# Kernel optimization log

Measured on AMD Instinct MI355X. Metric: run time of the kernel, lower is better.

## Reference

```python
import jax, jax.numpy as jnp
import numpy as np

B, S, E, H, NL = 64, 256, 1024, 16, 2
D = E // H          # head dim = 64
FF = 4 * E          # 4096
EPS = 1e-5
MASKED = -10000.0   # masked_bias buffer value


def layer_norm(x, g, b):
    m = jnp.mean(x, axis=-1, keepdims=True)
    v = jnp.mean(jnp.square(x - m), axis=-1, keepdims=True)
    return (x - m) * jax.lax.rsqrt(v + EPS) * g + b


def setup_inputs() -> dict:
    key = jax.random.key(0)
    ks = jax.random.split(key, 8)
    s = 0.02
    return {
        "sentence_hidden": jax.random.normal(ks[0], (B, S, E), dtype=jnp.float32),
        "wpe": jax.random.normal(ks[1], (256, E), dtype=jnp.float32) * s,
        "ln1_g": jnp.ones((NL, E), jnp.float32),
        "ln1_b": jnp.zeros((NL, E), jnp.float32),
        "attn_w": jax.random.normal(ks[2], (NL, E, 3 * E), dtype=jnp.float32) * s,
        "attn_b": jnp.zeros((NL, 3 * E), jnp.float32),
        "attn_proj_w": jax.random.normal(ks[3], (NL, E, E), dtype=jnp.float32) * s,
        "attn_proj_b": jnp.zeros((NL, E), jnp.float32),
        "ln2_g": jnp.ones((NL, E), jnp.float32),
        "ln2_b": jnp.zeros((NL, E), jnp.float32),
        "fc_w": jax.random.normal(ks[4], (NL, E, FF), dtype=jnp.float32) * s,
        "fc_b": jnp.zeros((NL, FF), jnp.float32),
        "mlp_proj_w": jax.random.normal(ks[5], (NL, FF, E), dtype=jnp.float32) * s,
        "mlp_proj_b": jnp.zeros((NL, E), jnp.float32),
        "lnf_g": jnp.ones((E,), jnp.float32),
        "lnf_b": jnp.zeros((E,), jnp.float32),
    }


def reference(sentence_hidden, wpe, ln1_g, ln1_b, attn_w, attn_b, attn_proj_w,
              attn_proj_b, ln2_g, ln2_b, fc_w, fc_b, mlp_proj_w, mlp_proj_b,
              lnf_g, lnf_b):
    # position embeddings: positions 0..S-1 (wpe has 256 rows, S == 256)
    h = sentence_hidden + wpe[:S][None, :, :]
    causal = jnp.tril(jnp.ones((S, S), dtype=bool))  # [S,S]
    scale = 1.0 / np.sqrt(D)
    for i in range(NL):
        # --- attention ---
        x = layer_norm(h, ln1_g[i], ln1_b[i])
        qkv = x @ attn_w[i] + attn_b[i]                    # [B,S,3E]
        q, k, v = jnp.split(qkv, 3, axis=-1)
        q = q.reshape(B, S, H, D).transpose(0, 2, 1, 3)    # [B,H,S,D]
        k = k.reshape(B, S, H, D).transpose(0, 2, 1, 3)
        v = v.reshape(B, S, H, D).transpose(0, 2, 1, 3)
        w = jnp.einsum("bhqd,bhkd->bhqk", q, k) * scale    # [B,H,S,S]
        w = jnp.where(causal, w, jnp.asarray(MASKED, w.dtype))
        w = jax.nn.softmax(w, axis=-1)
        a = jnp.einsum("bhqk,bhkd->bhqd", w, v)            # [B,H,S,D]
        a = a.transpose(0, 2, 1, 3).reshape(B, S, E)
        a = a @ attn_proj_w[i] + attn_proj_b[i]
        h = h + a
        # --- MLP ---
        x = layer_norm(h, ln2_g[i], ln2_b[i])
        m = jax.nn.gelu(x @ fc_w[i] + fc_b[i], approximate=True)  # gelu_new
        m = m @ mlp_proj_w[i] + mlp_proj_b[i]
        h = h + m
    h = layer_norm(h, lnf_g, lnf_b)
    loss = jnp.mean(jnp.square(h[0, :-1, :] - sentence_hidden[0, 1:, :]))
    return (h, loss)
```

## Files before the change

kernel.cpp:

```cpp
#include <hip/hip_runtime.h>
#include <cstdint>
#include <cstddef>


typedef __attribute__((ext_vector_type(4))) float f32x4;
typedef __attribute__((ext_vector_type(16))) float f32x16;
typedef __attribute__((ext_vector_type(8))) __bf16 bf16x8;
typedef __attribute__((ext_vector_type(4))) unsigned int u32x4;
typedef __attribute__((ext_vector_type(8))) unsigned short u16x8;
typedef __attribute__((ext_vector_type(4))) unsigned short u16x4;

__device__ __forceinline__ unsigned short f2bf(float x) {
  unsigned int u = __builtin_bit_cast(unsigned int, x);
  u += 0x7fffu + ((u >> 16) & 1u);
  return (unsigned short)(u >> 16);
}
__device__ __forceinline__ float gelu_new(float x) {
  float u = 0.7978845608028654f * (x + 0.044715f * x * x * x);
  return x * __builtin_amdgcn_rcpf(1.0f + __expf(-2.0f * u));
}
__device__ __forceinline__ unsigned int cvtpk(float lo, float hi) {
  unsigned int r;
  asm("v_cvt_pk_bf16_f32 %0, %1, %2" : "=v"(r) : "v"(lo), "v"(hi));
  return r;
}
__device__ __forceinline__ void plswap(unsigned int& a, unsigned int& b) {
  asm("v_permlane32_swap_b32 %0, %1" : "+v"(a), "+v"(b));
}

__global__ __launch_bounds__(256) void transpose_bf16(
    const float* __restrict__ W, unsigned short* __restrict__ Wt, int K, int N) {
  __shared__ float tile[32][33];
  const int n0 = blockIdx.x * 32, k0 = blockIdx.y * 32;
  const int tx = threadIdx.x, ty = threadIdx.y;
#pragma unroll
  for (int j = 0; j < 32; j += 8)
    tile[ty + j][tx] = W[(size_t)(k0 + ty + j) * N + n0 + tx];
  __syncthreads();
#pragma unroll
  for (int j = 0; j < 32; j += 8)
    Wt[(size_t)(n0 + ty + j) * K + k0 + tx] = f2bf(tile[tx][ty + j]);
}

__device__ __forceinline__ void ln_core(
    f32x4 v, const float* g, const float* bb, int row, int t,
    int outf32, void* outp) {
  float s = v.x + v.y + v.z + v.w;
  float sq = v.x * v.x + v.y * v.y + v.z * v.z + v.w * v.w;
#pragma unroll
  for (int off = 32; off; off >>= 1) {
    s += __shfl_xor(s, off, 64);
    sq += __shfl_xor(sq, off, 64);
  }
  __shared__ float red[8];
  if ((t & 63) == 0) { red[t >> 6] = s; red[4 + (t >> 6)] = sq; }
  __syncthreads();
  s = red[0] + red[1] + red[2] + red[3];
  sq = red[4] + red[5] + red[6] + red[7];
  const float mean = s * (1.0f / 1024.0f);
  const float var = sq * (1.0f / 1024.0f) - mean * mean;
  const float rs = rsqrtf(var + 1e-5f);
  const f32x4 gv = ((const f32x4*)g)[t];
  const f32x4 bv = ((const f32x4*)bb)[t];
  float y0 = (v.x - mean) * rs * gv.x + bv.x;
  float y1 = (v.y - mean) * rs * gv.y + bv.y;
  float y2 = (v.z - mean) * rs * gv.z + bv.z;
  float y3 = (v.w - mean) * rs * gv.w + bv.w;
  if (outf32) {
    f32x4 o; o.x = y0; o.y = y1; o.z = y2; o.w = y3;
    ((f32x4*)outp)[(size_t)row * 256 + t] = o;
  } else {
    u16x4 pk;
    pk.x = f2bf(y0); pk.y = f2bf(y1); pk.z = f2bf(y2); pk.w = f2bf(y3);
    ((u16x4*)outp)[(size_t)row * 256 + t] = pk;
  }
}

template <int OUTF32>
__global__ __launch_bounds__(256) void ln_kernel(
    const float* __restrict__ hin, const float* __restrict__ g,
    const float* __restrict__ bb, void* __restrict__ outp) {
  const int row = blockIdx.x, t = threadIdx.x;
  const f32x4 v = ((const f32x4*)(hin + (size_t)row * 1024))[t];
  ln_core(v, g, bb, row, t, OUTF32, outp);
}

__global__ __launch_bounds__(256) void ln_wpe_kernel(
    const float* __restrict__ sent, const float* __restrict__ wpe,
    const float* __restrict__ g, const float* __restrict__ bb,
    float* __restrict__ h, unsigned short* __restrict__ xb) {
  const int row = blockIdx.x, t = threadIdx.x;
  const int s = row & 255;
  f32x4 a = ((const f32x4*)(sent + (size_t)row * 1024))[t];
  f32x4 w = ((const f32x4*)(wpe + (size_t)s * 1024))[t];
  f32x4 v = a + w;
  ((f32x4*)(h + (size_t)row * 1024))[t] = v;
  ln_core(v, g, bb, row, t, 0, xb);
}

template <int EPI>
__global__ __launch_bounds__(512, 2) void gemmp(
    const unsigned short* __restrict__ A, const unsigned short* __restrict__ Bt,
    const float* __restrict__ bias, unsigned short* __restrict__ Cb,
    float* __restrict__ Hres, int N, int K, int gx, int gy) {
  constexpr int A_E = 16384;
  constexpr int BUF_E = A_E + 16384;
  __shared__ alignas(16) unsigned short smem[2 * BUF_E];

  const int nwg = gx * gy;
  const int dd = blockIdx.x;
  const int wrk = (dd & 7) * (nwg >> 3) + (dd >> 3);
  const int grp = wrk / (gx * 4);
  const int r = wrk - grp * (gx * 4);
  const int bx = r >> 2;
  const int by = grp * 4 + (r & 3);
  const int row0 = by * 256, col0 = bx * 256;

  const int t = threadIdx.x;
  const int wid = t >> 6, l = t & 63;
  const int wm = wid >> 2, wn = wid & 3;
  const int fr = l & 15, q4 = l >> 4;

  const int cx0 = (q4 ^ (fr & 7)) * 8;
  const int cx1 = ((4 + q4) ^ (fr & 7)) * 8;
  const int b_r0 = (wn * 64 + fr) * 64;
  auto a_slot = [&](int m) -> int { return (wm * 128 + m * 16 + fr) * 64; };

  const int lrow = l >> 3;
  const int scol = ((l & 7) ^ (lrow & 7)) * 8;

  auto stB = [&](int tt, int win) {
    const unsigned short* s =
        Bt + (size_t)(col0 + win * 8 + lrow) * K + tt * 64 + scol;
    __builtin_amdgcn_global_load_lds(
        (const __attribute__((address_space(1))) void*)s,
        (__attribute__((address_space(3))) void*)(smem + (tt & 1) * BUF_E + A_E + win * 512),
        16, 0, 0);
  };
  auto stA = [&](int tt, int win) {
    const unsigned short* s =
        A + (size_t)(row0 + win * 8 + lrow) * K + tt * 64 + scol;
    __builtin_amdgcn_global_load_lds(
        (const __attribute__((address_space(1))) void*)s,
        (__attribute__((address_space(3))) void*)(smem + (tt & 1) * BUF_E + win * 512),
        16, 0, 0);
  };
  auto stageB_set = [&](int tt) {
    stB(tt, 2 * wid); stB(tt, 2 * wid + 1);
    stB(tt, 16 + 2 * wid); stB(tt, 16 + 2 * wid + 1);
  };
  auto stageA_set = [&](int tt) {
    const int i0 = 2 * wid, i1 = 2 * wid + 1;
    stA(tt, i0 < 8 ? i0 : 8 + i0);
    stA(tt, i1 < 8 ? i1 : 8 + i1);
    stA(tt, i0 < 8 ? 8 + i0 : 16 + i0);
    stA(tt, i1 < 8 ? 8 + i1 : 16 + i1);
  };

  const int nt = K >> 6;

  stageB_set(0);
  stageA_set(0);
  asm volatile("s_waitcnt vmcnt(2)" ::: "memory");
  __builtin_amdgcn_s_barrier();
  asm volatile("" ::: "memory");

  f32x4 acc[8][4];
#pragma unroll
  for (int m = 0; m < 8; ++m)
#pragma unroll
    for (int n = 0; n < 4; ++n) {
      acc[m][n].x = 0.f; acc[m][n].y = 0.f; acc[m][n].z = 0.f; acc[m][n].w = 0.f;
    }

  for (int tc = 0; tc < nt; ++tc) {
    const unsigned short* Ab = smem + (tc & 1) * BUF_E;
    const unsigned short* Bb = Ab + A_E;
    const bool pf = (tc + 1) < nt;

    bf16x8 b0[4], b1[4], a0[4], a1[4];
#pragma unroll
    for (int n = 0; n < 4; ++n) b0[n] = *(const bf16x8*)(Bb + b_r0 + n * 1024 + cx0);
#pragma unroll
    for (int m = 0; m < 4; ++m) a0[m] = *(const bf16x8*)(Ab + a_slot(m) + cx0);
#pragma unroll
    for (int n = 0; n < 4; ++n) b1[n] = *(const bf16x8*)(Bb + b_r0 + n * 1024 + cx1);
#pragma unroll
    for (int m = 0; m < 4; ++m) a1[m] = *(const bf16x8*)(Ab + a_slot(m) + cx1);

    if (pf) stageB_set(tc + 1);

    __builtin_amdgcn_s_setprio(1);
#pragma unroll
    for (int m = 0; m < 4; ++m)
#pragma unroll
      for (int n = 0; n < 4; ++n)
        acc[m][n] = __builtin_amdgcn_mfma_f32_16x16x32_bf16(a0[m], b0[n], acc[m][n], 0, 0, 0);
    __builtin_amdgcn_s_setprio(0);

    if (pf) stageA_set(tc + 1);

    __builtin_amdgcn_s_setprio(1);
#pragma unroll
    for (int m = 0; m < 4; ++m)
#pragma unroll
      for (int n = 0; n < 4; ++n)
        acc[m][n] = __builtin_amdgcn_mfma_f32_16x16x32_bf16(a1[m], b1[n], acc[m][n], 0, 0, 0);
    __builtin_amdgcn_s_setprio(0);

    if (pf) asm volatile("s_waitcnt vmcnt(8)" ::: "memory");
    else    asm volatile("s_waitcnt vmcnt(0)" ::: "memory");
    __builtin_amdgcn_s_barrier();
    asm volatile("" ::: "memory");

    bf16x8 h0[4], h1[4];
#pragma unroll
    for (int m = 0; m < 4; ++m) h0[m] = *(const bf16x8*)(Ab + a_slot(4 + m) + cx0);
#pragma unroll
    for (int m = 0; m < 4; ++m) h1[m] = *(const bf16x8*)(Ab + a_slot(4 + m) + cx1);

    __builtin_amdgcn_s_setprio(1);
#pragma unroll
    for (int m = 0; m < 4; ++m)
#pragma unroll
      for (int n = 0; n < 4; ++n)
        acc[4 + m][n] = __builtin_amdgcn_mfma_f32_16x16x32_bf16(h0[m], b0[n], acc[4 + m][n], 0, 0, 0);
    __builtin_amdgcn_s_setprio(0);
    __builtin_amdgcn_s_setprio(1);
#pragma unroll
    for (int m = 0; m < 4; ++m)
#pragma unroll
      for (int n = 0; n < 4; ++n)
        acc[4 + m][n] = __builtin_amdgcn_mfma_f32_16x16x32_bf16(h1[m], b1[n], acc[4 + m][n], 0, 0, 0);
    __builtin_amdgcn_s_setprio(0);

    if (pf) asm volatile("s_waitcnt vmcnt(2)" ::: "memory");
    else    asm volatile("s_waitcnt vmcnt(0)" ::: "memory");
    __builtin_amdgcn_s_barrier();
    asm volatile("" ::: "memory");
  }

  if constexpr (EPI == 2) {
#pragma unroll
    for (int n = 0; n < 4; ++n) {
      const int col = col0 + wn * 64 + n * 16 + fr;
      const float bi = bias[col];
#pragma unroll
      for (int m = 0; m < 8; ++m)
#pragma unroll
        for (int e = 0; e < 4; ++e) {
          const int row = row0 + wm * 128 + m * 16 + q4 * 4 + e;
          Hres[(size_t)row * N + col] += acc[m][n][e] + bi;
        }
    }
  } else {
    char* wreg = (char*)smem + wid * 9216;
    float bi[4];
#pragma unroll
    for (int n = 0; n < 4; ++n) bi[n] = bias[col0 + wn * 64 + n * 16 + fr];
#pragma unroll
    for (int half = 0; half < 2; ++half) {
#pragma unroll
      for (int m = 0; m < 4; ++m)
#pragma unroll
        for (int n = 0; n < 4; ++n)
#pragma unroll
          for (int e = 0; e < 4; ++e) {
            float v = acc[half * 4 + m][n][e] + bi[n];
            if (EPI == 1) v = gelu_new(v);
            *(unsigned short*)(wreg + (m * 16 + q4 * 4 + e) * 144 +
                               (n * 16 + fr) * 2) = f2bf(v);
          }
#pragma unroll
      for (int rb = 0; rb < 8; ++rb) {
        const int rowl = rb * 8 + (l >> 3);
        u16x8 vv = *(const u16x8*)(wreg + rowl * 144 + (l & 7) * 16);
        const int rg = row0 + wm * 128 + half * 64 + rowl;
        *(u16x8*)(Cb + (size_t)rg * N + col0 + wn * 64 + (l & 7) * 8) = vv;
      }
    }
  }
}

__global__ __launch_bounds__(256) void attn_mfma(
    const unsigned short* __restrict__ qkv, unsigned short* __restrict__ aout,
    int b0) {
  __shared__ alignas(16) unsigned short Klds[256 * 64];
  __shared__ alignas(16) unsigned short Vt[64 * 256];
  const int bh = blockIdx.x;
  const int bl = bh >> 4, hd = bh & 15;
  const size_t base = (size_t)bl * 256 * 3072 + (size_t)hd * 64;
  const int t = threadIdx.x;
  const int w = t >> 6, l = t & 63;
  const int lq = l & 31, hl = l >> 5;

#pragma unroll
  for (int i = 0; i < 8; ++i) {
    const int r = i * 32 + (t >> 3);
    const int c = t & 7;
    u16x8 kv = *(const u16x8*)(qkv + base + (size_t)r * 3072 + 1024 + c * 8);
    *(u16x8*)(Klds + r * 64 + ((c ^ (r & 7)) * 8)) = kv;
    u16x8 vv = *(const u16x8*)(qkv + base + (size_t)r * 3072 + 2048 + c * 8);
#pragma unroll
    for (int j = 0; j < 8; ++j) {
      const int d = c * 8 + j;
      Vt[d * 256 + (((r >> 3) ^ (d & 31)) * 8) + (r & 7)] = vv[j];
    }
  }

  const int q0 = w * 64;
  bf16x8 qf[2][4];
#pragma unroll
  for (int n = 0; n < 2; ++n)
#pragma unroll
    for (int d16 = 0; d16 < 4; ++d16)
      qf[n][d16] = *(const bf16x8*)(qkv + base +
          (size_t)(q0 + n * 32 + lq) * 3072 + d16 * 16 + hl * 8);
  __syncthreads();

  const float cs = 0.125f * 1.44269504088896f;
  f32x16 O[2][2];
#pragma unroll
  for (int m = 0; m < 2; ++m)
#pragma unroll
    for (int n = 0; n < 2; ++n)
#pragma unroll
      for (int e = 0; e < 16; ++e) O[m][n][e] = 0.f;
  float mrun[2] = {-3.0e38f, -3.0e38f};
  float lrun[2] = {0.f, 0.f};

  const int ktmax = (q0 + 63) >> 5;
  for (int kt = 0; kt <= ktmax; ++kt) {
    bf16x8 kf[4];
    const int krow = kt * 32 + lq;
#pragma unroll
    for (int d16 = 0; d16 < 4; ++d16) {
      const int chunk = (d16 * 2 + hl) ^ (krow & 7);
      kf[d16] = *(const bf16x8*)(Klds + krow * 64 + chunk * 8);
    }
    const int nlo = (kt * 32 > q0 + 31) ? 1 : 0;
    bf16x8 pfrag[2][2];
#pragma unroll
    for (int n = 0; n < 2; ++n) {
      if (n < nlo) continue;
      f32x16 s;
#pragma unroll
      for (int e = 0; e < 16; ++e) s[e] = 0.f;
#pragma unroll
      for (int d16 = 0; d16 < 4; ++d16)
        s = __builtin_amdgcn_mfma_f32_32x32x16_bf16(kf[d16], qf[n][d16], s, 0, 0, 0);
      const int qg = q0 + n * 32 + lq;
      float sv[16];
#pragma unroll
      for (int r = 0; r < 16; ++r) {
        const int kg = kt * 32 + (r & 3) + 8 * (r >> 2) + 4 * hl;
        const float x = s[r] * cs;
        sv[r] = (kg > qg) ? -3.0e38f : x;
      }
      float pmax = sv[0];
#pragma unroll
      for (int r = 1; r < 16; ++r) pmax = fmaxf(pmax, sv[r]);
      pmax = fmaxf(pmax, __shfl_xor(pmax, 32, 64));
      const float nm = fmaxf(mrun[n], pmax);
      const float alpha = exp2f(mrun[n] - nm);
      mrun[n] = nm;
      float psum = 0.f;
#pragma unroll
      for (int r = 0; r < 16; ++r) {
        sv[r] = exp2f(sv[r] - nm);
        psum += sv[r];
      }
      psum += __shfl_xor(psum, 32, 64);
      lrun[n] = lrun[n] * alpha + psum;
#pragma unroll
      for (int m = 0; m < 2; ++m)
#pragma unroll
        for (int e = 0; e < 16; ++e) O[m][n][e] *= alpha;
#pragma unroll
      for (int h = 0; h < 2; ++h) {
        unsigned int a0 = cvtpk(sv[h * 8 + 0], sv[h * 8 + 1]);
        unsigned int a1 = cvtpk(sv[h * 8 + 2], sv[h * 8 + 3]);
        unsigned int c0 = cvtpk(sv[h * 8 + 4], sv[h * 8 + 5]);
        unsigned int c1 = cvtpk(sv[h * 8 + 6], sv[h * 8 + 7]);
        plswap(a0, c0);
        plswap(a1, c1);
        u32x4 fw; fw.x = a0; fw.y = a1; fw.z = c0; fw.w = c1;
        pfrag[n][h] = __builtin_bit_cast(bf16x8, fw);
      }
    }
#pragma unroll
    for (int m = 0; m < 2; ++m)
#pragma unroll
      for (int h = 0; h < 2; ++h) {
        const int dd = m * 32 + lq;
        const int chunk = (kt * 4 + h * 2 + hl) ^ (dd & 31);
        bf16x8 vf = *(const bf16x8*)(Vt + dd * 256 + chunk * 8);
#pragma unroll
        for (int n = 0; n < 2; ++n)
          if (n >= nlo)
            O[m][n] = __builtin_amdgcn_mfma_f32_32x32x16_bf16(vf, pfrag[n][h], O[m][n], 0, 0, 0);
      }
  }

#pragma unroll
  for (int n = 0; n < 2; ++n) {
    const float inv = 1.0f / lrun[n];
    const size_t row = (size_t)(b0 + bl) * 256 + q0 + n * 32 + lq;
#pragma unroll
    for (int m = 0; m < 2; ++m) {
#pragma unroll
      for (int qd = 0; qd < 4; ++qd) {
        u16x4 pk;
#pragma unroll
        for (int e = 0; e < 4; ++e) pk[e] = f2bf(O[m][n][qd * 4 + e] * inv);
        *(u16x4*)(aout + row * 1024 + hd * 64 + m * 32 + qd * 8 + hl * 4) = pk;
      }
    }
  }
}

__device__ __forceinline__ float block_reduce_sum256(float v) {
#pragma unroll
  for (int off = 32; off; off >>= 1) v += __shfl_xor(v, off, 64);
  __shared__ float red[4];
  const int t = threadIdx.x;
  if ((t & 63) == 0) red[t >> 6] = v;
  __syncthreads();
  return red[0] + red[1] + red[2] + red[3];
}

__global__ __launch_bounds__(256) void loss_partial(
    const float* __restrict__ hf, const float* __restrict__ sent,
    float* __restrict__ part) {
  const int s = blockIdx.x, t = threadIdx.x;
  f32x4 a = ((const f32x4*)(hf + (size_t)s * 1024))[t];
  f32x4 b = ((const f32x4*)(sent + (size_t)(s + 1) * 1024))[t];
  f32x4 d = a - b;
  float v = d.x * d.x + d.y * d.y + d.z * d.z + d.w * d.w;
  float tot = block_reduce_sum256(v);
  if (t == 0) part[s] = tot;
}

__global__ __launch_bounds__(256) void loss_final(
    const float* __restrict__ part, float* __restrict__ out) {
  const int t = threadIdx.x;
  float v = (t < 255) ? part[t] : 0.f;
  float s = block_reduce_sum256(v);
  if (t == 0) out[0] = s * (1.0f / (255.0f * 1024.0f));
}

constexpr size_t C_X     = 0;
constexpr size_t C_QKV   = 33554432;
constexpr size_t C_WQKV  = C_QKV + 67108864;
constexpr size_t C_WPROJ = C_WQKV + 6291456;
constexpr size_t C_WFC   = C_WPROJ + 2097152;
constexpr size_t C_WMLP  = C_WFC + 8388608;
constexpr size_t C_PART  = C_WMLP + 8388608;

constexpr size_t F_X     = 0;
constexpr size_t F_U     = 33554432;
constexpr size_t F_WQKV  = F_U + 134217728;
constexpr size_t F_WPROJ = F_WQKV + 6291456;
constexpr size_t F_WFC   = F_WPROJ + 2097152;
constexpr size_t F_WMLP  = F_WFC + 8388608;
constexpr size_t F_PART  = F_WMLP + 8388608;
constexpr size_t F_NEED  = F_PART + 4096;

extern "C" void kernel_launch(void* const* d_in, const int* in_sizes, int n_in,
                              void* d_out, int out_size, void* d_ws, size_t ws_size,
                              hipStream_t stream) {
  (void)in_sizes; (void)n_in; (void)out_size;
  const float* sent    = (const float*)d_in[0];
  const float* wpe     = (const float*)d_in[1];
  const float* ln1_g   = (const float*)d_in[2];
  const float* ln1_b   = (const float*)d_in[3];
  const float* attn_w  = (const float*)d_in[4];
  const float* attn_b  = (const float*)d_in[5];
  const float* attn_pw = (const float*)d_in[6];
  const float* attn_pb = (const float*)d_in[7];
  const float* ln2_g   = (const float*)d_in[8];
  const float* ln2_b   = (const float*)d_in[9];
  const float* fc_w    = (const float*)d_in[10];
  const float* fc_b    = (const float*)d_in[11];
  const float* mlp_w   = (const float*)d_in[12];
  const float* mlp_b   = (const float*)d_in[13];
  const float* lnf_g   = (const float*)d_in[14];
  const float* lnf_b   = (const float*)d_in[15];
  float* out_h = (float*)d_out;
  float* h = out_h;

  char* ws = (char*)d_ws;
  const bool fullm = ws_size >= F_NEED;

  unsigned short* xb    = (unsigned short*)(ws + (fullm ? F_X : C_X));
  unsigned short* ub    = (unsigned short*)(ws + (fullm ? F_U : C_QKV));
  unsigned short* wqkv  = (unsigned short*)(ws + (fullm ? F_WQKV : C_WQKV));
  unsigned short* wproj = (unsigned short*)(ws + (fullm ? F_WPROJ : C_WPROJ));
  unsigned short* wfc   = (unsigned short*)(ws + (fullm ? F_WFC : C_WFC));
  unsigned short* wmlp  = (unsigned short*)(ws + (fullm ? F_WMLP : C_WMLP));
  float* part           = (float*)(ws + (fullm ? F_PART : C_PART));

  const dim3 tb(32, 8, 1);
  for (int i = 0; i < 2; ++i) {
    transpose_bf16<<<dim3(96, 32), tb, 0, stream>>>(
        attn_w + (size_t)i * 1024 * 3072, wqkv, 1024, 3072);
    transpose_bf16<<<dim3(32, 32), tb, 0, stream>>>(
        attn_pw + (size_t)i * 1024 * 1024, wproj, 1024, 1024);
    transpose_bf16<<<dim3(128, 32), tb, 0, stream>>>(
        fc_w + (size_t)i * 1024 * 4096, wfc, 1024, 4096);
    transpose_bf16<<<dim3(32, 128), tb, 0, stream>>>(
        mlp_w + (size_t)i * 4096 * 1024, wmlp, 4096, 1024);

    if (i == 0)
      ln_wpe_kernel<<<16384, 256, 0, stream>>>(sent, wpe, ln1_g, ln1_b, h, xb);
    else
      ln_kernel<0><<<16384, 256, 0, stream>>>(h, ln1_g + i * 1024, ln1_b + i * 1024, xb);

    if (fullm) {
      gemmp<0><<<768, 512, 0, stream>>>(
          xb, wqkv, attn_b + i * 3072, ub, nullptr, 3072, 1024, 12, 64);
      attn_mfma<<<1024, 256, 0, stream>>>(ub, xb, 0);
    } else {
      for (int c = 0; c < 2; ++c) {
        const size_t r0 = (size_t)c * 8192;
        gemmp<0><<<384, 512, 0, stream>>>(
            xb + r0 * 1024, wqkv, attn_b + i * 3072, ub, nullptr, 3072, 1024, 12, 32);
        attn_mfma<<<512, 256, 0, stream>>>(ub, xb, c * 32);
      }
    }
    gemmp<2><<<256, 512, 0, stream>>>(
        xb, wproj, attn_pb + i * 1024, nullptr, h, 1024, 1024, 4, 64);

    ln_kernel<0><<<16384, 256, 0, stream>>>(h, ln2_g + i * 1024, ln2_b + i * 1024, xb);
    if (fullm) {
      gemmp<1><<<1024, 512, 0, stream>>>(
          xb, wfc, fc_b + i * 4096, ub, nullptr, 4096, 1024, 16, 64);
      gemmp<2><<<256, 512, 0, stream>>>(
          ub, wmlp, mlp_b + i * 1024, nullptr, h, 1024, 4096, 4, 64);
    } else {
      for (int c = 0; c < 2; ++c) {
        const size_t r0 = (size_t)c * 8192;
        gemmp<1><<<512, 512, 0, stream>>>(
            xb + r0 * 1024, wfc, fc_b + i * 4096, ub, nullptr, 4096, 1024, 16, 32);
        gemmp<2><<<128, 512, 0, stream>>>(
            ub, wmlp, mlp_b + i * 1024, nullptr, h + r0 * 1024, 1024, 4096, 4, 32);
      }
    }
  }

  ln_kernel<1><<<16384, 256, 0, stream>>>(h, lnf_g, lnf_b, out_h);
  loss_partial<<<255, 256, 0, stream>>>(out_h, sent, part);
  loss_final<<<1, 256, 0, stream>>>(part, out_h + 16777216);
}
```

Before: 1.138 ms.

## Use one-wave-per-row layernorm, 4x4 GEMM tile swizzle, and earlier A prefetch

Layernorm kernels now process one row per 64-lane wavefront, four rows per block. This drops the shared-memory reduction and block barrier and launches a quarter as many blocks. The GEMM block-to-tile mapping changes to 4x4 square clusters for better L2 reuse of A and B. The next A tile is now staged together with B before the first MFMA half, giving longer latency hiding at the cost of more outstanding loads and register pressure.

New measurement: 1.153 ms. Within noise of the previous version (+1.3%).

```diff
diff --git a/kernel.cpp b/kernel.cpp
--- a/kernel.cpp
+++ b/kernel.cpp
@@ -42,60 +42,90 @@
     Wt[(size_t)(n0 + ty + j) * K + k0 + tx] = f2bf(tile[tx][ty + j]);
 }
 
-__device__ __forceinline__ void ln_core(
-    f32x4 v, const float* g, const float* bb, int row, int t,
-    int outf32, void* outp) {
-  float s = v.x + v.y + v.z + v.w;
-  float sq = v.x * v.x + v.y * v.y + v.z * v.z + v.w * v.w;
+template <int OUTF32>
+__global__ __launch_bounds__(256) void ln4_kernel(
+    const float* __restrict__ hin, const float* __restrict__ g,
+    const float* __restrict__ bb, void* __restrict__ outp) {
+  const int lane = threadIdx.x & 63;
+  const int row = blockIdx.x * 4 + (threadIdx.x >> 6);
+  const f32x4* src = (const f32x4*)(hin + (size_t)row * 1024);
+  f32x4 v[4];
+#pragma unroll
+  for (int j = 0; j < 4; ++j) v[j] = src[j * 64 + lane];
+  float s = 0.f, sq = 0.f;
+#pragma unroll
+  for (int j = 0; j < 4; ++j) {
+    s += v[j].x + v[j].y + v[j].z + v[j].w;
+    sq += v[j].x * v[j].x + v[j].y * v[j].y + v[j].z * v[j].z + v[j].w * v[j].w;
+  }
 #pragma unroll
   for (int off = 32; off; off >>= 1) {
     s += __shfl_xor(s, off, 64);
     sq += __shfl_xor(sq, off, 64);
   }
-  __shared__ float red[8];
-  if ((t & 63) == 0) { red[t >> 6] = s; red[4 + (t >> 6)] = sq; }
-  __syncthreads();
-  s = red[0] + red[1] + red[2] + red[3];
-  sq = red[4] + red[5] + red[6] + red[7];
   const float mean = s * (1.0f / 1024.0f);
   const float var = sq * (1.0f / 1024.0f) - mean * mean;
   const float rs = rsqrtf(var + 1e-5f);
-  const f32x4 gv = ((const f32x4*)g)[t];
-  const f32x4 bv = ((const f32x4*)bb)[t];
-  float y0 = (v.x - mean) * rs * gv.x + bv.x;
-  float y1 = (v.y - mean) * rs * gv.y + bv.y;
-  float y2 = (v.z - mean) * rs * gv.z + bv.z;
-  float y3 = (v.w - mean) * rs * gv.w + bv.w;
-  if (outf32) {
-    f32x4 o; o.x = y0; o.y = y1; o.z = y2; o.w = y3;
-    ((f32x4*)outp)[(size_t)row * 256 + t] = o;
-  } else {
-    u16x4 pk;
-    pk.x = f2bf(y0); pk.y = f2bf(y1); pk.z = f2bf(y2); pk.w = f2bf(y3);
-    ((u16x4*)outp)[(size_t)row * 256 + t] = pk;
-  }
-}
-
-template <int OUTF32>
-__global__ __launch_bounds__(256) void ln_kernel(
-    const float* __restrict__ hin, const float* __restrict__ g,
-    const float* __restrict__ bb, void* __restrict__ outp) {
-  const int row = blockIdx.x, t = threadIdx.x;
-  const f32x4 v = ((const f32x4*)(hin + (size_t)row * 1024))[t];
-  ln_core(v, g, bb, row, t, OUTF32, outp);
-}
-
-__global__ __launch_bounds__(256) void ln_wpe_kernel(
+#pragma unroll
+  for (int j = 0; j < 4; ++j) {
+    const f32x4 gv = ((const f32x4*)g)[j * 64 + lane];
+    const f32x4 bv = ((const f32x4*)bb)[j * 64 + lane];
+    float y0 = (v[j].x - mean) * rs * gv.x + bv.x;
+    float y1 = (v[j].y - mean) * rs * gv.y + bv.y;
+    float y2 = (v[j].z - mean) * rs * gv.z + bv.z;
+    float y3 = (v[j].w - mean) * rs * gv.w + bv.w;
+    if (OUTF32) {
+      f32x4 o; o.x = y0; o.y = y1; o.z = y2; o.w = y3;
+      ((f32x4*)outp)[(size_t)row * 256 + j * 64 + lane] = o;
+    } else {
+      u16x4 pk;
+      pk.x = f2bf(y0); pk.y = f2bf(y1); pk.z = f2bf(y2); pk.w = f2bf(y3);
+      ((u16x4*)outp)[(size_t)row * 256 + j * 64 + lane] = pk;
+    }
+  }
+}
+
+__global__ __launch_bounds__(256) void ln4_wpe_kernel(
     const float* __restrict__ sent, const float* __restrict__ wpe,
     const float* __restrict__ g, const float* __restrict__ bb,
     float* __restrict__ h, unsigned short* __restrict__ xb) {
-  const int row = blockIdx.x, t = threadIdx.x;
-  const int s = row & 255;
-  f32x4 a = ((const f32x4*)(sent + (size_t)row * 1024))[t];
-  f32x4 w = ((const f32x4*)(wpe + (size_t)s * 1024))[t];
-  f32x4 v = a + w;
-  ((f32x4*)(h + (size_t)row * 1024))[t] = v;
-  ln_core(v, g, bb, row, t, 0, xb);
+  const int lane = threadIdx.x & 63;
+  const int row = blockIdx.x * 4 + (threadIdx.x >> 6);
+  const int sp = row & 255;
+  const f32x4* src = (const f32x4*)(sent + (size_t)row * 1024);
+  const f32x4* wp = (const f32x4*)(wpe + (size_t)sp * 1024);
+  f32x4* hp = (f32x4*)(h + (size_t)row * 1024);
+  f32x4 v[4];
+#pragma unroll
+  for (int j = 0; j < 4; ++j) {
+    v[j] = src[j * 64 + lane] + wp[j * 64 + lane];
+    hp[j * 64 + lane] = v[j];
+  }
+  float s = 0.f, sq = 0.f;
+#pragma unroll
+  for (int j = 0; j < 4; ++j) {
+    s += v[j].x + v[j].y + v[j].z + v[j].w;
+    sq += v[j].x * v[j].x + v[j].y * v[j].y + v[j].z * v[j].z + v[j].w * v[j].w;
+  }
+#pragma unroll
+  for (int off = 32; off; off >>= 1) {
+    s += __shfl_xor(s, off, 64);
+    sq += __shfl_xor(sq, off, 64);
+  }
+  const float mean = s * (1.0f / 1024.0f);
+  const float var = sq * (1.0f / 1024.0f) - mean * mean;
+  const float rs = rsqrtf(var + 1e-5f);
+#pragma unroll
+  for (int j = 0; j < 4; ++j) {
+    const f32x4 gv = ((const f32x4*)g)[j * 64 + lane];
+    const f32x4 bv = ((const f32x4*)bb)[j * 64 + lane];
+    u16x4 pk;
+    pk.x = f2bf((v[j].x - mean) * rs * gv.x + bv.x);
+    pk.y = f2bf((v[j].y - mean) * rs * gv.y + bv.y);
+    pk.z = f2bf((v[j].z - mean) * rs * gv.z + bv.z);
+    pk.w = f2bf((v[j].w - mean) * rs * gv.w + bv.w);
+    ((u16x4*)xb)[(size_t)row * 256 + j * 64 + lane] = pk;
+  }
 }
 
 template <int EPI>
@@ -110,10 +140,13 @@
   const int nwg = gx * gy;
   const int dd = blockIdx.x;
   const int wrk = (dd & 7) * (nwg >> 3) + (dd >> 3);
-  const int grp = wrk / (gx * 4);
-  const int r = wrk - grp * (gx * 4);
-  const int bx = r >> 2;
-  const int by = grp * 4 + (r & 3);
+  const int cid = wrk >> 4;
+  const int cin = wrk & 15;
+  const int cpr = gx >> 2;
+  const int cby = cid / cpr;
+  const int cbx = cid - cby * cpr;
+  const int bx = cbx * 4 + (cin & 3);
+  const int by = cby * 4 + (cin >> 2);
   const int row0 = by * 256, col0 = bx * 256;
 
   const int t = threadIdx.x;
@@ -188,7 +221,7 @@
 #pragma unroll
     for (int m = 0; m < 4; ++m) a1[m] = *(const bf16x8*)(Ab + a_slot(m) + cx1);
 
-    if (pf) stageB_set(tc + 1);
+    if (pf) { stageB_set(tc + 1); stageA_set(tc + 1); }
 
     __builtin_amdgcn_s_setprio(1);
 #pragma unroll
@@ -197,8 +230,6 @@
       for (int n = 0; n < 4; ++n)
         acc[m][n] = __builtin_amdgcn_mfma_f32_16x16x32_bf16(a0[m], b0[n], acc[m][n], 0, 0, 0);
     __builtin_amdgcn_s_setprio(0);
-
-    if (pf) stageA_set(tc + 1);
 
     __builtin_amdgcn_s_setprio(1);
 #pragma unroll
@@ -512,9 +543,9 @@
         mlp_w + (size_t)i * 4096 * 1024, wmlp, 4096, 1024);
 
     if (i == 0)
-      ln_wpe_kernel<<<16384, 256, 0, stream>>>(sent, wpe, ln1_g, ln1_b, h, xb);
+      ln4_wpe_kernel<<<4096, 256, 0, stream>>>(sent, wpe, ln1_g, ln1_b, h, xb);
     else
-      ln_kernel<0><<<16384, 256, 0, stream>>>(h, ln1_g + i * 1024, ln1_b + i * 1024, xb);
+      ln4_kernel<0><<<4096, 256, 0, stream>>>(h, ln1_g + i * 1024, ln1_b + i * 1024, xb);
 
     if (fullm) {
       gemmp<0><<<768, 512, 0, stream>>>(
@@ -531,7 +562,7 @@
     gemmp<2><<<256, 512, 0, stream>>>(
         xb, wproj, attn_pb + i * 1024, nullptr, h, 1024, 1024, 4, 64);
 
-    ln_kernel<0><<<16384, 256, 0, stream>>>(h, ln2_g + i * 1024, ln2_b + i * 1024, xb);
+    ln4_kernel<0><<<4096, 256, 0, stream>>>(h, ln2_g + i * 1024, ln2_b + i * 1024, xb);
     if (fullm) {
       gemmp<1><<<1024, 512, 0, stream>>>(
           xb, wfc, fc_b + i * 4096, ub, nullptr, 4096, 1024, 16, 64);
@@ -548,7 +579,7 @@
     }
   }
 
-  ln_kernel<1><<<16384, 256, 0, stream>>>(h, lnf_g, lnf_b, out_h);
+  ln4_kernel<1><<<4096, 256, 0, stream>>>(h, lnf_g, lnf_b, out_h);
   loss_partial<<<255, 256, 0, stream>>>(out_h, sent, part);
   loss_final<<<1, 256, 0, stream>>>(part, out_h + 16777216);
 }
```
